# Kernel optimization log

Measured on AMD Instinct MI355X. Metric: run time of the kernel, lower is better.

## Reference

```python
import jax, jax.numpy as jnp
import numpy as np

BS, T, HS, WS = 2, 4, 32, 32
HW = HS * WS
D, NH, NL, NP = 256, 8, 4, 4
HD = D // NH
DFFN = 1024


def layer_norm(x, g, b, eps=1e-5):
    mu = jnp.mean(x, axis=-1, keepdims=True)
    var = jnp.mean((x - mu) ** 2, axis=-1, keepdims=True)
    return (x - mu) * jax.lax.rsqrt(var + eps) * g + b


def bilinear_gather(val, loc, Hl, Wl):
    # val: (bs, nh, Hl*Wl, hd); loc: (bs, Lq, nh, P, 2) in [0,1], last dim (x, y)
    # matches F.grid_sample(align_corners=False, padding_mode='zeros') on grid=2*loc-1
    x = loc[..., 0] * Wl - 0.5
    y = loc[..., 1] * Hl - 0.5
    x0 = jnp.floor(x)
    y0 = jnp.floor(y)
    lx = x - x0
    ly = y - y0
    bs, Lq, nh, P = x.shape
    out = jnp.zeros((bs, nh, Lq * P, val.shape[-1]), val.dtype)
    for dy in (0, 1):
        for dx in (0, 1):
            xi = x0 + dx
            yi = y0 + dy
            w = (lx if dx else 1.0 - lx) * (ly if dy else 1.0 - ly)
            valid = (xi >= 0) & (xi < Wl) & (yi >= 0) & (yi < Hl)
            w = jnp.where(valid, w, 0.0)
            xi_c = jnp.clip(xi, 0, Wl - 1).astype(jnp.int32)
            yi_c = jnp.clip(yi, 0, Hl - 1).astype(jnp.int32)
            idx = (yi_c * Wl + xi_c).transpose(0, 2, 1, 3).reshape(bs, nh, Lq * P)
            g = jnp.take_along_axis(val, idx[..., None], axis=2)
            wt = w.transpose(0, 2, 1, 3).reshape(bs, nh, Lq * P)
            out = out + wt[..., None] * g
    return out.reshape(bs, nh, Lq, P, val.shape[-1])


def setup_inputs() -> dict:
    key = jax.random.key(0)
    ks = jax.random.split(key, 12)
    s = 0.02
    return {
        "src": jax.random.normal(ks[0], (BS, T, HW, D), jnp.float32),
        "pos": jax.random.normal(ks[1], (BS, T, HW, D), jnp.float32),
        "reference_points": jax.random.uniform(ks[2], (BS, T * HW, NL, 2), jnp.float32),
        "value_proj_w": jax.random.normal(ks[3], (D, D), jnp.float32) * s,
        "value_proj_b": jnp.zeros((D,), jnp.float32),
        "sampling_offsets_w": jax.random.normal(ks[4], (D, NH * NL * NP * 2), jnp.float32) * s,
        "sampling_offsets_b": jax.random.normal(ks[5], (NH * NL * NP * 2,), jnp.float32) * s,
        "attn_weights_w": jax.random.normal(ks[6], (D, NH * NL * NP), jnp.float32) * s,
        "attn_weights_b": jnp.zeros((NH * NL * NP,), jnp.float32),
        "output_proj_w": jax.random.normal(ks[7], (D, D), jnp.float32) * s,
        "output_proj_b": jnp.zeros((D,), jnp.float32),
        "norm1_g": jnp.ones((D,), jnp.float32),
        "norm1_b": jnp.zeros((D,), jnp.float32),
        "linear1_w": jax.random.normal(ks[8], (D, DFFN), jnp.float32) * s,
        "linear1_b": jnp.zeros((DFFN,), jnp.float32),
        "linear2_w": jax.random.normal(ks[9], (DFFN, D), jnp.float32) * s,
        "linear2_b": jnp.zeros((D,), jnp.float32),
        "norm2_g": jnp.ones((D,), jnp.float32),
        "norm2_b": jnp.zeros((D,), jnp.float32),
        "spatial_shapes": np.array([[HS, WS]] * NL, np.int32),
        "level_start_index": np.arange(NL, dtype=np.int32) * HW,
    }


def reference(src, pos, reference_points, value_proj_w, value_proj_b,
              sampling_offsets_w, sampling_offsets_b, attn_weights_w, attn_weights_b,
              output_proj_w, output_proj_b, norm1_g, norm1_b,
              linear1_w, linear1_b, linear2_w, linear2_b, norm2_g, norm2_b,
              spatial_shapes, level_start_index):
    bs, t, hw, d = src.shape
    Lq = t * hw
    x = src.reshape(bs, Lq, d)
    q = x  # module never adds pos in forward (with_pos_embed unused)
    value = (x @ value_proj_w + value_proj_b).reshape(bs, Lq, NH, HD)
    offsets = (q @ sampling_offsets_w + sampling_offsets_b).reshape(bs, Lq, NH, NL, NP, 2)
    aw = jax.nn.softmax((q @ attn_weights_w + attn_weights_b).reshape(bs, Lq, NH, NL * NP), axis=-1)
    aw = aw.reshape(bs, Lq, NH, NL, NP)
    ss = np.asarray(spatial_shapes)
    lsi = np.asarray(level_start_index)
    offset_normalizer = jnp.asarray(ss[:, ::-1].copy(), src.dtype)  # (L, 2) = (W, H)
    sampling_locations = reference_points[:, :, None, :, None, :] + offsets / offset_normalizer[None, None, None, :, None, :]
    attn_out = jnp.zeros((bs, NH, Lq, HD), src.dtype)
    for l in range(NL):
        Hl, Wl = int(ss[l, 0]), int(ss[l, 1])
        start = int(lsi[l])
        v_l = value[:, start:start + Hl * Wl].transpose(0, 2, 1, 3)  # (bs, nh, HlWl, hd)
        samp = bilinear_gather(v_l, sampling_locations[:, :, :, l], Hl, Wl)  # (bs, nh, Lq, P, hd)
        w_l = aw[:, :, :, l].transpose(0, 2, 1, 3)  # (bs, nh, Lq, P)
        attn_out = attn_out + jnp.sum(samp * w_l[..., None], axis=3)
    attn_out = attn_out.transpose(0, 2, 1, 3).reshape(bs, Lq, d) @ output_proj_w + output_proj_b
    x = layer_norm(x + attn_out, norm1_g, norm1_b)
    ffn = jax.nn.relu(x @ linear1_w + linear1_b) @ linear2_w + linear2_b
    x = layer_norm(x + ffn, norm2_g, norm2_b)
    return x.reshape(bs, t, hw, d), sampling_locations
```

## Files before the change

kernel.cpp:

```cpp
#include <hip/hip_runtime.h>
#include <math.h>

#define ROWS   8192
#define LQ     4096
#define NHEAD  8
#define NLVL   4
#define NPTS   4
#define HDIM   32

typedef __attribute__((ext_vector_type(8))) short v8s;
typedef __attribute__((ext_vector_type(4))) float v4f;

__device__ __forceinline__ unsigned short f2bf(float x) {
    unsigned int u = __float_as_uint(x);
    u += 0x7fffu + ((u >> 16) & 1u);
    return (unsigned short)(u >> 16);
}
__device__ __forceinline__ float bf2f(unsigned short x) {
    return __uint_as_float(((unsigned int)x) << 16);
}

__device__ __forceinline__ void glds16(const void* g, void* l) {
    __builtin_amdgcn_global_load_lds(
        (const __attribute__((address_space(1))) unsigned int*)g,
        (__attribute__((address_space(3))) unsigned int*)l, 16, 0, 0);
}

__device__ __forceinline__ void trans_tile(const float* __restrict__ in,
                                           unsigned short* __restrict__ out,
                                           int K, int N, int ldout, int n_off,
                                           int bx, int by, int tid)
{
    __shared__ float t[32][33];
    int tx = tid & 31, ty = tid >> 5;
    int k0 = by << 5, n0 = bx << 5;
    #pragma unroll
    for (int i = 0; i < 4; i++)
        t[ty + i * 8][tx] = in[(size_t)(k0 + ty + i * 8) * N + n0 + tx];
    __syncthreads();
    #pragma unroll
    for (int i = 0; i < 4; i++)
        out[(size_t)(n_off + n0 + ty + i * 8) * ldout + k0 + tx] = f2bf(t[tx][ty + i * 8]);
}

__global__ __launch_bounds__(256) void prep_k(
    const float* __restrict__ src, unsigned short* __restrict__ src_bf,
    const float* __restrict__ vw, const float* __restrict__ ofw,
    const float* __restrict__ aww, const float* __restrict__ pw,
    const float* __restrict__ w1, const float* __restrict__ w2,
    unsigned short* __restrict__ Btcat, unsigned short* __restrict__ pwT,
    unsigned short* __restrict__ w1T, unsigned short* __restrict__ w2T,
    const float* __restrict__ vb, const float* __restrict__ ofb,
    const float* __restrict__ awb, float* __restrict__ biascat)
{
    int bid = blockIdx.x, tid = threadIdx.x;
    if (bid < 2048) {
        int i = bid * 256 + tid;
        float4 v = ((const float4*)src)[i];
        ushort4 o;
        o.x = f2bf(v.x); o.y = f2bf(v.y); o.z = f2bf(v.z); o.w = f2bf(v.w);
        ((ushort4*)src_bf)[i] = o;
    } else if (bid < 2112) {
        int t = bid - 2048; trans_tile(vw, Btcat, 256, 256, 256, 0, t & 7, t >> 3, tid);
    } else if (bid < 2176) {
        int t = bid - 2112; trans_tile(ofw, Btcat, 256, 256, 256, 256, t & 7, t >> 3, tid);
    } else if (bid < 2208) {
        int t = bid - 2176; trans_tile(aww, Btcat, 256, 128, 256, 512, t & 3, t >> 2, tid);
    } else if (bid < 2272) {
        int t = bid - 2208; trans_tile(pw, pwT, 256, 256, 256, 0, t & 7, t >> 3, tid);
    } else if (bid < 2528) {
        int t = bid - 2272; trans_tile(w1, w1T, 256, 1024, 256, 0, t & 31, t >> 5, tid);
    } else if (bid < 2784) {
        int t = bid - 2528; trans_tile(w2, w2T, 1024, 256, 1024, 0, t & 7, t >> 3, tid);
    } else {
        biascat[tid] = vb[tid];
        biascat[tid + 256] = ofb[tid];
        if (tid < 128) biascat[tid + 512] = awb[tid];
    }
}

template<bool PROJ, bool OUTBF, bool RELU, bool RES>
__global__ __launch_bounds__(256) void mfma_gemm_k(
    const unsigned short* __restrict__ A,
    const unsigned short* __restrict__ Bt,
    const float* __restrict__ bias,
    const float* __restrict__ res,
    void* __restrict__ Cout,
    unsigned short* __restrict__ vbf,
    const float* __restrict__ refp,
    float* __restrict__ oloc,
    int M, int N, int K)
{
    __shared__ __align__(16) unsigned short As[4096];
    __shared__ __align__(16) unsigned short Bs[2048];
    const int tid = threadIdx.x;
    const int row0 = blockIdx.y << 7, col0 = blockIdx.x << 6;
    const int wid = tid >> 6, lane = tid & 63;
    const int wm = wid & 1, wn = wid >> 1;
    const int lr = lane & 15, kq = lane >> 4;

    v4f acc[4][2];
    #pragma unroll
    for (int i = 0; i < 4; i++)
        #pragma unroll
        for (int j = 0; j < 2; j++) acc[i][j] = (v4f){0.f, 0.f, 0.f, 0.f};

    for (int k0 = 0; k0 < K; k0 += 32) {
        __syncthreads();
        #pragma unroll
        for (int i = 0; i < 2; i++) {
            int c = wid * 128 + i * 64 + lane;
            int row = c >> 2;
            int kk = ((c & 3) + (row >> 2)) & 3;
            glds16(A + (size_t)(row0 + row) * K + k0 + kk * 8,
                   &As[(wid * 128 + i * 64) * 8]);
        }
        {
            int c = wid * 64 + lane;
            int row = c >> 2;
            int kk = ((c & 3) + (row >> 2)) & 3;
            glds16(Bt + (size_t)(col0 + row) * K + k0 + kk * 8,
                   &Bs[wid * 512]);
        }
        __syncthreads();
        v8s bf[2];
        #pragma unroll
        for (int nt = 0; nt < 2; nt++) {
            int row = wn * 32 + nt * 16 + lr;
            int s = (kq - (row >> 2)) & 3;
            bf[nt] = *(const v8s*)(&Bs[(row * 4 + s) * 8]);
        }
        #pragma unroll
        for (int mt = 0; mt < 4; mt++) {
            int row = wm * 64 + mt * 16 + lr;
            int s = (kq - (row >> 2)) & 3;
            v8s af = *(const v8s*)(&As[(row * 4 + s) * 8]);
            #pragma unroll
            for (int nt = 0; nt < 2; nt++)
                acc[mt][nt] = __builtin_amdgcn_mfma_f32_16x16x32_bf16(af, bf[nt], acc[mt][nt], 0, 0, 0);
        }
    }

    const int rq = lane >> 4;
    #pragma unroll
    for (int mt = 0; mt < 4; mt++) {
        #pragma unroll
        for (int nt = 0; nt < 2; nt++) {
            int col = col0 + wn * 32 + nt * 16 + lr;
            float bv = bias[col];
            #pragma unroll
            for (int i = 0; i < 4; i++) {
                int row = row0 + wm * 64 + mt * 16 + rq * 4 + i;
                float v = acc[mt][nt][i] + bv;
                if (RELU) v = fmaxf(v, 0.f);
                if (RES)  v += res[(size_t)row * N + col];
                if (PROJ) {
                    if (col0 < 256) {
                        int b = row >> 12, rb = row & 4095;
                        int l = rb >> 10, pix = rb & 1023;
                        int h = col >> 5, d = col & 31;
                        size_t idx = ((size_t)(((b << 2) + l) * 8 + h) << 15) + (pix << 5) + d;
                        vbf[idx] = f2bf(v);
                    } else if (col0 < 512) {
                        int colm = col - 256;
                        int l = (colm >> 3) & 3, cc = colm & 1;
                        oloc[(size_t)row * 256 + colm] =
                            refp[(size_t)row * 8 + l * 2 + cc] + v * (1.f / 32.f);
                    } else {
                        ((float*)Cout)[(size_t)row * 128 + col - 512] = v;
                    }
                } else if (OUTBF) {
                    ((unsigned short*)Cout)[(size_t)row * N + col] = f2bf(v);
                } else {
                    ((float*)Cout)[(size_t)row * N + col] = v;
                }
            }
        }
    }
}

template<bool OUTBF, bool RELU, bool RES>
__global__ __launch_bounds__(256) void mfma_gemm64_k(
    const unsigned short* __restrict__ A,
    const unsigned short* __restrict__ Bt,
    const float* __restrict__ bias,
    const float* __restrict__ res,
    void* __restrict__ Cout,
    int M, int N, int K)
{
    __shared__ __align__(16) unsigned short As[2048];
    __shared__ __align__(16) unsigned short Bs[2048];
    const int tid = threadIdx.x;
    const int row0 = blockIdx.y << 6, col0 = blockIdx.x << 6;
    const int wid = tid >> 6, lane = tid & 63;
    const int lr = lane & 15, kq = lane >> 4;

    v4f acc[4];
    #pragma unroll
    for (int i = 0; i < 4; i++) acc[i] = (v4f){0.f, 0.f, 0.f, 0.f};

    for (int k0 = 0; k0 < K; k0 += 32) {
        __syncthreads();
        {
            int c = wid * 64 + lane;
            int row = c >> 2;
            int kk = ((c & 3) + (row >> 2)) & 3;
            glds16(A + (size_t)(row0 + row) * K + k0 + kk * 8, &As[wid * 512]);
            glds16(Bt + (size_t)(col0 + row) * K + k0 + kk * 8, &Bs[wid * 512]);
        }
        __syncthreads();
        int colr = wid * 16 + lr;
        int sb = (kq - (colr >> 2)) & 3;
        v8s bf = *(const v8s*)(&Bs[(colr * 4 + sb) * 8]);
        #pragma unroll
        for (int mt = 0; mt < 4; mt++) {
            int rowr = mt * 16 + lr;
            int sa = (kq - (rowr >> 2)) & 3;
            v8s af = *(const v8s*)(&As[(rowr * 4 + sa) * 8]);
            acc[mt] = __builtin_amdgcn_mfma_f32_16x16x32_bf16(af, bf, acc[mt], 0, 0, 0);
        }
    }

    const int rq = lane >> 4;
    const int col = col0 + wid * 16 + lr;
    float bv = bias[col];
    #pragma unroll
    for (int mt = 0; mt < 4; mt++) {
        #pragma unroll
        for (int i = 0; i < 4; i++) {
            int row = row0 + mt * 16 + rq * 4 + i;
            float v = acc[mt][i] + bv;
            if (RELU) v = fmaxf(v, 0.f);
            if (RES)  v += res[(size_t)row * N + col];
            if (OUTBF) ((unsigned short*)Cout)[(size_t)row * N + col] = f2bf(v);
            else       ((float*)Cout)[(size_t)row * N + col] = v;
        }
    }
}

__global__ __launch_bounds__(256) void fused_gather_k(
    const float* __restrict__ po,
    const unsigned short* __restrict__ vbf,
    const float* __restrict__ loc,
    unsigned short* __restrict__ attn_bf)
{
    int tid = threadIdx.x;
    int u = tid >> 5, l = (tid >> 3) & 3, d4 = tid & 7;
    int h = blockIdx.x & 7;
    int r = (blockIdx.x >> 3) * 8 + u;
    int b = r >> 12;

    float locv[8];
    *(float4*)(locv)     = *(const float4*)(loc + (size_t)r * 256 + h * 32 + l * 8);
    *(float4*)(locv + 4) = *(const float4*)(loc + (size_t)r * 256 + h * 32 + l * 8 + 4);

    float w4[4];
    *(float4*)(w4) = *(const float4*)(po + (size_t)r * 128 + h * 16 + l * 4);
    float m = fmaxf(fmaxf(w4[0], w4[1]), fmaxf(w4[2], w4[3]));
    m = fmaxf(m, __shfl_xor(m, 8));
    m = fmaxf(m, __shfl_xor(m, 16));
    float s = 0.f;
    #pragma unroll
    for (int p = 0; p < 4; p++) { w4[p] = __expf(w4[p] - m); s += w4[p]; }
    s += __shfl_xor(s, 8);
    s += __shfl_xor(s, 16);
    float inv = 1.f / s;

    const unsigned short* vbase =
        vbf + (((size_t)(((b << 2) + l) * 8 + h)) << 15) + d4 * 4;
    ushort4 uv[16];
    float cw[16];
    #pragma unroll
    for (int p = 0; p < 4; p++) {
        float xf = locv[p * 2] * 32.f - 0.5f, yf = locv[p * 2 + 1] * 32.f - 0.5f;
        float x0f = floorf(xf), y0f = floorf(yf);
        float fx = xf - x0f, fy = yf - y0f;
        int x0 = (int)x0f, y0 = (int)y0f;
        float wgt = w4[p] * inv;
        #pragma unroll
        for (int dy = 0; dy < 2; dy++) {
            #pragma unroll
            for (int dx = 0; dx < 2; dx++) {
                int idx = p * 4 + dy * 2 + dx;
                int xi = x0 + dx, yi = y0 + dy;
                float wt = (dx ? fx : 1.f - fx) * (dy ? fy : 1.f - fy);
                bool valid = (xi >= 0) & (xi < 32) & (yi >= 0) & (yi < 32);
                int xc = min(max(xi, 0), 31), yc = min(max(yi, 0), 31);
                cw[idx] = valid ? (wgt * wt) : 0.f;
                uv[idx] = *(const ushort4*)(vbase + (size_t)((yc << 5) + xc) * 32);
            }
        }
    }
    float4 acc = {0.f, 0.f, 0.f, 0.f};
    #pragma unroll
    for (int idx = 0; idx < 16; idx++) {
        float c = cw[idx];
        acc.x += c * bf2f(uv[idx].x); acc.y += c * bf2f(uv[idx].y);
        acc.z += c * bf2f(uv[idx].z); acc.w += c * bf2f(uv[idx].w);
    }
    acc.x += __shfl_xor(acc.x, 8);  acc.y += __shfl_xor(acc.y, 8);
    acc.z += __shfl_xor(acc.z, 8);  acc.w += __shfl_xor(acc.w, 8);
    acc.x += __shfl_xor(acc.x, 16); acc.y += __shfl_xor(acc.y, 16);
    acc.z += __shfl_xor(acc.z, 16); acc.w += __shfl_xor(acc.w, 16);
    if (l == 0) {
        ushort4 o;
        o.x = f2bf(acc.x); o.y = f2bf(acc.y); o.z = f2bf(acc.z); o.w = f2bf(acc.w);
        *(ushort4*)(attn_bf + (size_t)r * 256 + h * 32 + d4 * 4) = o;
    }
}

template<bool WRITE_BF>
__global__ __launch_bounds__(256) void layernorm_k(
    float* __restrict__ x, const float* __restrict__ g, const float* __restrict__ b,
    unsigned short* __restrict__ xbf)
{
    int lane = threadIdx.x & 63;
    int wv = threadIdx.x >> 6;
    int row = blockIdx.x * 4 + wv;
    int c = lane << 2;
    float4 v = *(const float4*)(x + (size_t)row * 256 + c);
    float s = v.x + v.y + v.z + v.w;
    #pragma unroll
    for (int o = 1; o < 64; o <<= 1) s += __shfl_xor(s, o);
    float mu = s * (1.f / 256.f);
    float d0 = v.x - mu, d1 = v.y - mu, d2 = v.z - mu, d3 = v.w - mu;
    float vs = d0 * d0 + d1 * d1 + d2 * d2 + d3 * d3;
    #pragma unroll
    for (int o = 1; o < 64; o <<= 1) vs += __shfl_xor(vs, o);
    float rstd = rsqrtf(vs * (1.f / 256.f) + 1e-5f);
    float4 gg = *(const float4*)(g + c);
    float4 bb = *(const float4*)(b + c);
    float4 o4;
    o4.x = d0 * rstd * gg.x + bb.x;
    o4.y = d1 * rstd * gg.y + bb.y;
    o4.z = d2 * rstd * gg.z + bb.z;
    o4.w = d3 * rstd * gg.w + bb.w;
    *(float4*)(x + (size_t)row * 256 + c) = o4;
    if (WRITE_BF) {
        ushort4 ob;
        ob.x = f2bf(o4.x); ob.y = f2bf(o4.y); ob.z = f2bf(o4.z); ob.w = f2bf(o4.w);
        *(ushort4*)(xbf + (size_t)row * 256 + c) = ob;
    }
}

extern "C" void kernel_launch(void* const* d_in, const int* in_sizes, int n_in,
                              void* d_out, int out_size, void* d_ws, size_t ws_size,
                              hipStream_t stream)
{
    const float* src   = (const float*)d_in[0];
    const float* refp  = (const float*)d_in[2];
    const float* vw    = (const float*)d_in[3];
    const float* vb    = (const float*)d_in[4];
    const float* ofw   = (const float*)d_in[5];
    const float* ofb   = (const float*)d_in[6];
    const float* aww   = (const float*)d_in[7];
    const float* awb   = (const float*)d_in[8];
    const float* pw    = (const float*)d_in[9];
    const float* pb    = (const float*)d_in[10];
    const float* g1    = (const float*)d_in[11];
    const float* b1    = (const float*)d_in[12];
    const float* w1    = (const float*)d_in[13];
    const float* bi1   = (const float*)d_in[14];
    const float* w2    = (const float*)d_in[15];
    const float* bi2   = (const float*)d_in[16];
    const float* g2    = (const float*)d_in[17];
    const float* b2    = (const float*)d_in[18];

    float* ws = (float*)d_ws;
    float*          po        = ws;
    float*          x1        = ws + 1048576;
    unsigned short* value_bf  = (unsigned short*)(ws + 3145728);
    unsigned short* src_bf    = (unsigned short*)(ws + 4194304);
    unsigned short* x1_bf     = (unsigned short*)(ws + 5242880);
    unsigned short* attn_bf   = (unsigned short*)(ws + 6291456);
    unsigned short* hidden_bf = (unsigned short*)(ws + 7340032);
    unsigned short* Btcat     = (unsigned short*)(ws + 11534336);
    unsigned short* pwT       = (unsigned short*)(ws + 11616256);
    unsigned short* w1T       = (unsigned short*)(ws + 11649024);
    unsigned short* w2T       = (unsigned short*)(ws + 11780096);
    float*          biascat   = ws + 11911168;

    float* out_x   = (float*)d_out;
    float* out_loc = out_x + 2097152;

    dim3 blk(256);

    prep_k<<<2785, blk, 0, stream>>>(src, src_bf, vw, ofw, aww, pw, w1, w2,
                                     Btcat, pwT, w1T, w2T, vb, ofb, awb, biascat);

    mfma_gemm_k<true, false, false, false><<<dim3(10, 64), blk, 0, stream>>>(
        src_bf, Btcat, biascat, nullptr, po, value_bf, refp, out_loc, ROWS, 640, 256);

    fused_gather_k<<<8192, blk, 0, stream>>>(po, value_bf, out_loc, attn_bf);

    mfma_gemm64_k<false, false, true><<<dim3(4, 128), blk, 0, stream>>>(
        attn_bf, pwT, pb, src, x1, ROWS, 256, 256);
    layernorm_k<true><<<2048, blk, 0, stream>>>(x1, g1, b1, x1_bf);

    mfma_gemm_k<false, true, true, false><<<dim3(16, 64), blk, 0, stream>>>(
        x1_bf, w1T, bi1, nullptr, hidden_bf, nullptr, nullptr, nullptr, ROWS, 1024, 256);
    mfma_gemm64_k<false, false, true><<<dim3(4, 128), blk, 0, stream>>>(
        hidden_bf, w2T, bi2, x1, out_x, ROWS, 256, 1024);
    layernorm_k<false><<<2048, blk, 0, stream>>>(out_x, g2, b2, nullptr);
}
```

Measured before the change: 189.2 us.

## Fuse LayerNorm into output-projection and FFN2 GEMM epilogues

Replaces the 64x64-tile residual GEMM plus separate LayerNorm kernel with one kernel where each block computes a full 32x256 row tile and applies LayerNorm in the epilogue. Row statistics are reduced via shuffles and a small shared-memory table, and single-pass variance (E[x^2]-mu^2) is used. This removes two kernel launches and a full read/write pass of the activation buffer per LayerNorm. In exchange, grid size drops to 256 blocks, reducing parallelism and latency hiding, and the single-pass variance is slightly less numerically robust.

```diff
diff --git a/kernel.cpp b/kernel.cpp
--- a/kernel.cpp
+++ b/kernel.cpp
@@ -179,61 +179,138 @@
     }
 }
 
-template<bool OUTBF, bool RELU, bool RES>
-__global__ __launch_bounds__(256) void mfma_gemm64_k(
+template<bool WRITE_BF>
+__global__ __launch_bounds__(256) void mfma_gemm_ln_k(
     const unsigned short* __restrict__ A,
     const unsigned short* __restrict__ Bt,
     const float* __restrict__ bias,
     const float* __restrict__ res,
-    void* __restrict__ Cout,
-    int M, int N, int K)
-{
-    __shared__ __align__(16) unsigned short As[2048];
-    __shared__ __align__(16) unsigned short Bs[2048];
+    const float* __restrict__ g,
+    const float* __restrict__ b,
+    float* __restrict__ out,
+    unsigned short* __restrict__ outbf,
+    int M, int K)
+{
+    __shared__ __align__(16) unsigned short As[1024];
+    __shared__ __align__(16) unsigned short Bs[8192];
+    __shared__ float red[2][32][4];
     const int tid = threadIdx.x;
-    const int row0 = blockIdx.y << 6, col0 = blockIdx.x << 6;
+    const int row0 = blockIdx.x << 5;
     const int wid = tid >> 6, lane = tid & 63;
     const int lr = lane & 15, kq = lane >> 4;
-
-    v4f acc[4];
-    #pragma unroll
-    for (int i = 0; i < 4; i++) acc[i] = (v4f){0.f, 0.f, 0.f, 0.f};
+    const int rq = kq;
+
+    v4f acc[2][4];
+    #pragma unroll
+    for (int i = 0; i < 2; i++)
+        #pragma unroll
+        for (int j = 0; j < 4; j++) acc[i][j] = (v4f){0.f, 0.f, 0.f, 0.f};
 
     for (int k0 = 0; k0 < K; k0 += 32) {
         __syncthreads();
-        {
+        if (wid < 2) {
             int c = wid * 64 + lane;
             int row = c >> 2;
             int kk = ((c & 3) + (row >> 2)) & 3;
-            glds16(A + (size_t)(row0 + row) * K + k0 + kk * 8, &As[wid * 512]);
-            glds16(Bt + (size_t)(col0 + row) * K + k0 + kk * 8, &Bs[wid * 512]);
+            glds16(A + (size_t)(row0 + row) * K + k0 + kk * 8,
+                   &As[(wid * 64) * 8]);
+        }
+        #pragma unroll
+        for (int i = 0; i < 4; i++) {
+            int c = (wid * 4 + i) * 64 + lane;
+            int col = c >> 2;
+            int kk = ((c & 3) + (col >> 2)) & 3;
+            glds16(Bt + (size_t)col * K + k0 + kk * 8,
+                   &Bs[((wid * 4 + i) * 64) * 8]);
         }
         __syncthreads();
-        int colr = wid * 16 + lr;
-        int sb = (kq - (colr >> 2)) & 3;
-        v8s bf = *(const v8s*)(&Bs[(colr * 4 + sb) * 8]);
-        #pragma unroll
-        for (int mt = 0; mt < 4; mt++) {
-            int rowr = mt * 16 + lr;
-            int sa = (kq - (rowr >> 2)) & 3;
-            v8s af = *(const v8s*)(&As[(rowr * 4 + sa) * 8]);
-            acc[mt] = __builtin_amdgcn_mfma_f32_16x16x32_bf16(af, bf, acc[mt], 0, 0, 0);
-        }
-    }
-
-    const int rq = lane >> 4;
-    const int col = col0 + wid * 16 + lr;
-    float bv = bias[col];
-    #pragma unroll
-    for (int mt = 0; mt < 4; mt++) {
+        v8s bf[4];
+        #pragma unroll
+        for (int ct = 0; ct < 4; ct++) {
+            int col = wid * 64 + ct * 16 + lr;
+            int s = (kq - (col >> 2)) & 3;
+            bf[ct] = *(const v8s*)(&Bs[(col * 4 + s) * 8]);
+        }
+        #pragma unroll
+        for (int rt = 0; rt < 2; rt++) {
+            int rowl = rt * 16 + lr;
+            int s = (kq - (rowl >> 2)) & 3;
+            v8s af = *(const v8s*)(&As[(rowl * 4 + s) * 8]);
+            #pragma unroll
+            for (int ct = 0; ct < 4; ct++)
+                acc[rt][ct] = __builtin_amdgcn_mfma_f32_16x16x32_bf16(af, bf[ct], acc[rt][ct], 0, 0, 0);
+        }
+    }
+
+    float t[2][4][4];
+    float s1[2][4], s2[2][4];
+    #pragma unroll
+    for (int rt = 0; rt < 2; rt++)
+        #pragma unroll
+        for (int i = 0; i < 4; i++) { s1[rt][i] = 0.f; s2[rt][i] = 0.f; }
+    #pragma unroll
+    for (int rt = 0; rt < 2; rt++) {
+        #pragma unroll
+        for (int ct = 0; ct < 4; ct++) {
+            int col = wid * 64 + ct * 16 + lr;
+            float bv = bias[col];
+            #pragma unroll
+            for (int i = 0; i < 4; i++) {
+                int row = row0 + rt * 16 + rq * 4 + i;
+                float v = acc[rt][ct][i] + bv + res[(size_t)row * 256 + col];
+                t[rt][ct][i] = v;
+                s1[rt][i] += v;
+                s2[rt][i] += v * v;
+            }
+        }
+    }
+    #pragma unroll
+    for (int o = 1; o < 16; o <<= 1) {
+        #pragma unroll
+        for (int rt = 0; rt < 2; rt++)
+            #pragma unroll
+            for (int i = 0; i < 4; i++) {
+                s1[rt][i] += __shfl_xor(s1[rt][i], o);
+                s2[rt][i] += __shfl_xor(s2[rt][i], o);
+            }
+    }
+    if (lr == 0) {
+        #pragma unroll
+        for (int rt = 0; rt < 2; rt++)
+            #pragma unroll
+            for (int i = 0; i < 4; i++) {
+                int rl = rt * 16 + rq * 4 + i;
+                red[0][rl][wid] = s1[rt][i];
+                red[1][rl][wid] = s2[rt][i];
+            }
+    }
+    __syncthreads();
+    float mu[2][4], rstd[2][4];
+    #pragma unroll
+    for (int rt = 0; rt < 2; rt++) {
         #pragma unroll
         for (int i = 0; i < 4; i++) {
-            int row = row0 + mt * 16 + rq * 4 + i;
-            float v = acc[mt][i] + bv;
-            if (RELU) v = fmaxf(v, 0.f);
-            if (RES)  v += res[(size_t)row * N + col];
-            if (OUTBF) ((unsigned short*)Cout)[(size_t)row * N + col] = f2bf(v);
-            else       ((float*)Cout)[(size_t)row * N + col] = v;
+            int rl = rt * 16 + rq * 4 + i;
+            float S1 = red[0][rl][0] + red[0][rl][1] + red[0][rl][2] + red[0][rl][3];
+            float S2 = red[1][rl][0] + red[1][rl][1] + red[1][rl][2] + red[1][rl][3];
+            float m = S1 * (1.f / 256.f);
+            mu[rt][i] = m;
+            rstd[rt][i] = rsqrtf(S2 * (1.f / 256.f) - m * m + 1e-5f);
+        }
+    }
+    #pragma unroll
+    for (int rt = 0; rt < 2; rt++) {
+        #pragma unroll
+        for (int ct = 0; ct < 4; ct++) {
+            int col = wid * 64 + ct * 16 + lr;
+            float gg = g[col], bb = b[col];
+            #pragma unroll
+            for (int i = 0; i < 4; i++) {
+                int row = row0 + rt * 16 + rq * 4 + i;
+                float o = (t[rt][ct][i] - mu[rt][i]) * rstd[rt][i] * gg + bb;
+                out[(size_t)row * 256 + col] = o;
+                if (WRITE_BF) outbf[(size_t)row * 256 + col] = f2bf(o);
+            }
         }
     }
 }
@@ -306,40 +383,6 @@
         ushort4 o;
         o.x = f2bf(acc.x); o.y = f2bf(acc.y); o.z = f2bf(acc.z); o.w = f2bf(acc.w);
         *(ushort4*)(attn_bf + (size_t)r * 256 + h * 32 + d4 * 4) = o;
-    }
-}
-
-template<bool WRITE_BF>
-__global__ __launch_bounds__(256) void layernorm_k(
-    float* __restrict__ x, const float* __restrict__ g, const float* __restrict__ b,
-    unsigned short* __restrict__ xbf)
-{
-    int lane = threadIdx.x & 63;
-    int wv = threadIdx.x >> 6;
-    int row = blockIdx.x * 4 + wv;
-    int c = lane << 2;
-    float4 v = *(const float4*)(x + (size_t)row * 256 + c);
-    float s = v.x + v.y + v.z + v.w;
-    #pragma unroll
-    for (int o = 1; o < 64; o <<= 1) s += __shfl_xor(s, o);
-    float mu = s * (1.f / 256.f);
-    float d0 = v.x - mu, d1 = v.y - mu, d2 = v.z - mu, d3 = v.w - mu;
-    float vs = d0 * d0 + d1 * d1 + d2 * d2 + d3 * d3;
-    #pragma unroll
-    for (int o = 1; o < 64; o <<= 1) vs += __shfl_xor(vs, o);
-    float rstd = rsqrtf(vs * (1.f / 256.f) + 1e-5f);
-    float4 gg = *(const float4*)(g + c);
-    float4 bb = *(const float4*)(b + c);
-    float4 o4;
-    o4.x = d0 * rstd * gg.x + bb.x;
-    o4.y = d1 * rstd * gg.y + bb.y;
-    o4.z = d2 * rstd * gg.z + bb.z;
-    o4.w = d3 * rstd * gg.w + bb.w;
-    *(float4*)(x + (size_t)row * 256 + c) = o4;
-    if (WRITE_BF) {
-        ushort4 ob;
-        ob.x = f2bf(o4.x); ob.y = f2bf(o4.y); ob.z = f2bf(o4.z); ob.w = f2bf(o4.w);
-        *(ushort4*)(xbf + (size_t)row * 256 + c) = ob;
     }
 }
 
@@ -393,13 +436,12 @@
 
     fused_gather_k<<<8192, blk, 0, stream>>>(po, value_bf, out_loc, attn_bf);
 
-    mfma_gemm64_k<false, false, true><<<dim3(4, 128), blk, 0, stream>>>(
-        attn_bf, pwT, pb, src, x1, ROWS, 256, 256);
-    layernorm_k<true><<<2048, blk, 0, stream>>>(x1, g1, b1, x1_bf);
+    mfma_gemm_ln_k<true><<<256, blk, 0, stream>>>(
+        attn_bf, pwT, pb, src, g1, b1, x1, x1_bf, ROWS, 256);
 
     mfma_gemm_k<false, true, true, false><<<dim3(16, 64), blk, 0, stream>>>(
         x1_bf, w1T, bi1, nullptr, hidden_bf, nullptr, nullptr, nullptr, ROWS, 1024, 256);
-    mfma_gemm64_k<false, false, true><<<dim3(4, 128), blk, 0, stream>>>(
-        hidden_bf, w2T, bi2, x1, out_x, ROWS, 256, 1024);
-    layernorm_k<false><<<2048, blk, 0, stream>>>(out_x, g2, b2, nullptr);
-}
+
+    mfma_gemm_ln_k<false><<<256, blk, 0, stream>>>(
+        hidden_bf, w2T, bi2, x1, g2, b2, out_x, nullptr, ROWS, 1024);
+}
```

New measurement: 195.4 us. +3.3%, slower.

## Stage per-level value maps in LDS for deformable gather, reduce levels separately

Applied to the files above, without the earlier changes.

Replaces the global-memory bilinear gather with a kernel where each block copies one (batch, level, head) 1024x32 bf16 value map (64 KB) into LDS, then serves 512 query rows from it. Per-level partial sums go to a new fp32 workspace buffer, and a second kernel adds the four levels and converts to bf16. The goal is to turn scattered global reads into LDS reads. The cost is an extra 8 MB fp32 write and read, another launch, and only 512 blocks, each holding 64 KB of LDS, which limits occupancy.

```diff
diff --git a/kernel.cpp b/kernel.cpp
--- a/kernel.cpp
+++ b/kernel.cpp
@@ -238,75 +238,95 @@
     }
 }
 
-__global__ __launch_bounds__(256) void fused_gather_k(
+__global__ __launch_bounds__(256) void gather_lds_k(
     const float* __restrict__ po,
     const unsigned short* __restrict__ vbf,
     const float* __restrict__ loc,
-    unsigned short* __restrict__ attn_bf)
-{
-    int tid = threadIdx.x;
-    int u = tid >> 5, l = (tid >> 3) & 3, d4 = tid & 7;
-    int h = blockIdx.x & 7;
-    int r = (blockIdx.x >> 3) * 8 + u;
-    int b = r >> 12;
-
-    float locv[8];
-    *(float4*)(locv)     = *(const float4*)(loc + (size_t)r * 256 + h * 32 + l * 8);
-    *(float4*)(locv + 4) = *(const float4*)(loc + (size_t)r * 256 + h * 32 + l * 8 + 4);
-
-    float w4[4];
-    *(float4*)(w4) = *(const float4*)(po + (size_t)r * 128 + h * 16 + l * 4);
-    float m = fmaxf(fmaxf(w4[0], w4[1]), fmaxf(w4[2], w4[3]));
-    m = fmaxf(m, __shfl_xor(m, 8));
-    m = fmaxf(m, __shfl_xor(m, 16));
-    float s = 0.f;
-    #pragma unroll
-    for (int p = 0; p < 4; p++) { w4[p] = __expf(w4[p] - m); s += w4[p]; }
-    s += __shfl_xor(s, 8);
-    s += __shfl_xor(s, 16);
-    float inv = 1.f / s;
-
-    const unsigned short* vbase =
-        vbf + (((size_t)(((b << 2) + l) * 8 + h)) << 15) + d4 * 4;
-    ushort4 uv[16];
-    float cw[16];
-    #pragma unroll
-    for (int p = 0; p < 4; p++) {
-        float xf = locv[p * 2] * 32.f - 0.5f, yf = locv[p * 2 + 1] * 32.f - 0.5f;
-        float x0f = floorf(xf), y0f = floorf(yf);
-        float fx = xf - x0f, fy = yf - y0f;
-        int x0 = (int)x0f, y0 = (int)y0f;
-        float wgt = w4[p] * inv;
-        #pragma unroll
-        for (int dy = 0; dy < 2; dy++) {
+    float* __restrict__ part)
+{
+    int bid = blockIdx.x, tid = threadIdx.x;
+    int h = bid & 7, rc = (bid >> 3) & 7, l = (bid >> 6) & 3, b = bid >> 8;
+
+    __shared__ __align__(16) unsigned short vt[32768];
+
+    const unsigned short* vsub = vbf + (((size_t)(((b << 2) + l) * 8 + h)) << 15);
+    int wv = tid >> 6, lane = tid & 63;
+    #pragma unroll
+    for (int i = 0; i < 16; i++) {
+        int base = i * 256 + wv * 64;
+        glds16(vsub + (size_t)(base + lane) * 8, &vt[base * 8]);
+    }
+    __syncthreads();
+
+    int g = tid >> 3, d4 = tid & 7;
+    int rbase = b * 4096 + rc * 512;
+    #pragma unroll 2
+    for (int i = 0; i < 16; i++) {
+        int r = rbase + g + i * 32;
+        float2 lg = *(const float2*)(po + (size_t)r * 128 + h * 16 + d4 * 2);
+        float m = fmaxf(lg.x, lg.y);
+        m = fmaxf(m, __shfl_xor(m, 1, 8));
+        m = fmaxf(m, __shfl_xor(m, 2, 8));
+        m = fmaxf(m, __shfl_xor(m, 4, 8));
+        float e0 = __expf(lg.x - m), e1 = __expf(lg.y - m);
+        float s = e0 + e1;
+        s += __shfl_xor(s, 1, 8);
+        s += __shfl_xor(s, 2, 8);
+        s += __shfl_xor(s, 4, 8);
+        float inv = 1.f / s;
+        float ww0 = e0 * inv, ww1 = e1 * inv;
+        float wgt[4];
+        wgt[0] = __shfl(ww0, l * 2, 8);
+        wgt[1] = __shfl(ww1, l * 2, 8);
+        wgt[2] = __shfl(ww0, l * 2 + 1, 8);
+        wgt[3] = __shfl(ww1, l * 2 + 1, 8);
+
+        float locv[8];
+        *(float4*)(locv)     = *(const float4*)(loc + (size_t)r * 256 + h * 32 + l * 8);
+        *(float4*)(locv + 4) = *(const float4*)(loc + (size_t)r * 256 + h * 32 + l * 8 + 4);
+
+        float a0 = 0.f, a1 = 0.f, a2 = 0.f, a3 = 0.f;
+        #pragma unroll
+        for (int p = 0; p < 4; p++) {
+            float xf = locv[p * 2] * 32.f - 0.5f, yf = locv[p * 2 + 1] * 32.f - 0.5f;
+            float x0f = floorf(xf), y0f = floorf(yf);
+            float fx = xf - x0f, fy = yf - y0f;
+            int x0 = (int)x0f, y0 = (int)y0f;
             #pragma unroll
-            for (int dx = 0; dx < 2; dx++) {
-                int idx = p * 4 + dy * 2 + dx;
-                int xi = x0 + dx, yi = y0 + dy;
-                float wt = (dx ? fx : 1.f - fx) * (dy ? fy : 1.f - fy);
-                bool valid = (xi >= 0) & (xi < 32) & (yi >= 0) & (yi < 32);
-                int xc = min(max(xi, 0), 31), yc = min(max(yi, 0), 31);
-                cw[idx] = valid ? (wgt * wt) : 0.f;
-                uv[idx] = *(const ushort4*)(vbase + (size_t)((yc << 5) + xc) * 32);
+            for (int dy = 0; dy < 2; dy++) {
+                #pragma unroll
+                for (int dx = 0; dx < 2; dx++) {
+                    int xi = x0 + dx, yi = y0 + dy;
+                    float wt = (dx ? fx : 1.f - fx) * (dy ? fy : 1.f - fy);
+                    bool valid = (xi >= 0) & (xi < 32) & (yi >= 0) & (yi < 32);
+                    int xc = min(max(xi, 0), 31), yc = min(max(yi, 0), 31);
+                    float c = valid ? (wgt[p] * wt) : 0.f;
+                    ushort4 u = *(const ushort4*)(&vt[((yc << 5) + xc) * 32 + d4 * 4]);
+                    a0 += c * bf2f(u.x); a1 += c * bf2f(u.y);
+                    a2 += c * bf2f(u.z); a3 += c * bf2f(u.w);
+                }
             }
         }
-    }
-    float4 acc = {0.f, 0.f, 0.f, 0.f};
-    #pragma unroll
-    for (int idx = 0; idx < 16; idx++) {
-        float c = cw[idx];
-        acc.x += c * bf2f(uv[idx].x); acc.y += c * bf2f(uv[idx].y);
-        acc.z += c * bf2f(uv[idx].z); acc.w += c * bf2f(uv[idx].w);
-    }
-    acc.x += __shfl_xor(acc.x, 8);  acc.y += __shfl_xor(acc.y, 8);
-    acc.z += __shfl_xor(acc.z, 8);  acc.w += __shfl_xor(acc.w, 8);
-    acc.x += __shfl_xor(acc.x, 16); acc.y += __shfl_xor(acc.y, 16);
-    acc.z += __shfl_xor(acc.z, 16); acc.w += __shfl_xor(acc.w, 16);
-    if (l == 0) {
-        ushort4 o;
-        o.x = f2bf(acc.x); o.y = f2bf(acc.y); o.z = f2bf(acc.z); o.w = f2bf(acc.w);
-        *(ushort4*)(attn_bf + (size_t)r * 256 + h * 32 + d4 * 4) = o;
-    }
+        float4 o = {a0, a1, a2, a3};
+        *(float4*)(part + (size_t)l * 2097152 + (size_t)r * 256 + h * 32 + d4 * 4) = o;
+    }
+}
+
+__global__ __launch_bounds__(256) void reduce_k(
+    const float* __restrict__ part, unsigned short* __restrict__ attn_bf)
+{
+    int i = blockIdx.x * 256 + threadIdx.x;
+    const float4* p = (const float4*)part;
+    float4 a = p[i];
+    float4 b = p[i + 524288];
+    float4 c = p[i + 1048576];
+    float4 d = p[i + 1572864];
+    ushort4 o;
+    o.x = f2bf(a.x + b.x + c.x + d.x);
+    o.y = f2bf(a.y + b.y + c.y + d.y);
+    o.z = f2bf(a.z + b.z + c.z + d.z);
+    o.w = f2bf(a.w + b.w + c.w + d.w);
+    ((ushort4*)attn_bf)[i] = o;
 }
 
 template<bool WRITE_BF>
@@ -379,6 +399,7 @@
     unsigned short* w1T       = (unsigned short*)(ws + 11649024);
     unsigned short* w2T       = (unsigned short*)(ws + 11780096);
     float*          biascat   = ws + 11911168;
+    float*          part      = ws + 11912192;
 
     float* out_x   = (float*)d_out;
     float* out_loc = out_x + 2097152;
@@ -391,7 +412,8 @@
     mfma_gemm_k<true, false, false, false><<<dim3(10, 64), blk, 0, stream>>>(
         src_bf, Btcat, biascat, nullptr, po, value_bf, refp, out_loc, ROWS, 640, 256);
 
-    fused_gather_k<<<8192, blk, 0, stream>>>(po, value_bf, out_loc, attn_bf);
+    gather_lds_k<<<512, blk, 0, stream>>>(po, value_bf, out_loc, part);
+    reduce_k<<<2048, blk, 0, stream>>>(part, attn_bf);
 
     mfma_gemm64_k<false, false, true><<<dim3(4, 128), blk, 0, stream>>>(
         attn_bf, pwT, pb, src, x1, ROWS, 256, 256);
```

After: 196.9 us. +4.1%, slower.
